# Optimization experiments

Measured on AMD Instinct MI355X. Metric: run time of the kernel, lower is better.

## Reference

```python
import jax, jax.numpy as jnp
import numpy as np

FACTOR = 5.0
SCALE = 1.0 / np.sqrt(FACTOR)  # module uses scale or 1/sqrt(factor), NOT 1/sqrt(E)


def setup_inputs() -> dict:
    key = jax.random.key(0)
    k1, k2, k3, k4 = jax.random.split(key, 4)
    B, H, L, S, E = 8, 8, 1024, 1024, 64
    queries = jax.random.normal(k1, (B, H, L, E), dtype=jnp.float32)
    keys = jax.random.normal(k2, (B, H, S, E), dtype=jnp.float32)
    values = jax.random.normal(k3, (B, H, S, E), dtype=jnp.float32)
    time_diffs = jax.random.uniform(k4, (B, L), dtype=jnp.float32)  # non-negative time gaps
    return {"queries": queries, "keys": keys, "values": values, "time_diffs": time_diffs}


def reference(queries, keys, values, time_diffs):
    # decay: [B, 1, L, 1] multiplicative bias on raw scores (pre-scale, pre-softmax)
    decay = jnp.exp(-time_diffs / FACTOR)[:, None, :, None]
    scores = jnp.einsum('bhle,bhse->bhls', queries, keys) * decay  # [B,H,L,S]
    A = jax.nn.softmax(SCALE * scores, axis=-1)
    V = jnp.einsum('bhls,bhse->bhle', A, values)
    return V
```

## Files before the change

kernel.cpp:

```cpp
#include <hip/hip_runtime.h>
#include <hip/hip_bf16.h>


#define Lq   1024
#define Sk   1024
#define Ed   64
#define QBLK 128
#define KVBLK 64
#define NT   (Sk / KVBLK)
#define NBH  64

typedef __attribute__((ext_vector_type(8)))  short          short8;
typedef __attribute__((ext_vector_type(8)))  unsigned short ushort8;
typedef __attribute__((ext_vector_type(4)))  float          f32x4;
typedef __attribute__((ext_vector_type(16))) float          f32x16;
typedef __attribute__((ext_vector_type(4)))  unsigned int   uint4v;

__device__ __forceinline__ unsigned short f2bf(float x) {
    unsigned int u = __float_as_uint(x);
    u += 0x7FFFu + ((u >> 16) & 1u);
    return (unsigned short)(u >> 16);
}

__device__ __forceinline__ unsigned cvt_pk_bf16(float lo, float hi) {
    unsigned r;
    asm("v_cvt_pk_bf16_f32 %0, %1, %2" : "=v"(r) : "v"(lo), "v"(hi));
    return r;
}

__device__ __forceinline__ void gl_lds16(const void* g, void* lds) {
    __builtin_amdgcn_global_load_lds(
        (const __attribute__((address_space(1))) void*)g,
        (__attribute__((address_space(3))) void*)lds, 16, 0, 0);
}

__global__ __launch_bounds__(256) void prep_kv(const float* __restrict__ K,
                                               const float* __restrict__ V,
                                               unsigned short* __restrict__ Kb,
                                               unsigned short* __restrict__ Vt) {
    int bid = blockIdx.x;
    if (bid < 2048) {
        int gid = bid * 256 + threadIdx.x;
        int row = gid >> 3;
        int jb  = gid & 7;
        const float* src = K + (size_t)row * Ed + jb * 8;
        float4 a = *(const float4*)src;
        float4 c = *(const float4*)(src + 4);
        ushort8 w;
        w[0]=f2bf(a.x); w[1]=f2bf(a.y); w[2]=f2bf(a.z); w[3]=f2bf(a.w);
        w[4]=f2bf(c.x); w[5]=f2bf(c.y); w[6]=f2bf(c.z); w[7]=f2bf(c.w);
        *(ushort8*)(Kb + (size_t)row * Ed + ((jb ^ (row & 7)) << 3)) = w;
    } else {
        int vb  = bid - 2048;
        int bh  = vb >> 4;
        int kv0 = (vb & 15) * KVBLK;
        int e   = threadIdx.x & 63;
        int jh  = threadIdx.x >> 6;
        const float* Vg = V + (size_t)bh * Sk * Ed;
        unsigned short* Vo = Vt + (size_t)bh * Ed * Sk;
        #pragma unroll
        for (int half = 0; half < 2; ++half) {
            int jb = jh + half * 4;
            ushort8 w;
            #pragma unroll
            for (int i = 0; i < 8; ++i)
                w[i] = f2bf(Vg[(size_t)(kv0 + jb * 8 + i) * Ed + e]);
            *(ushort8*)(Vo + (size_t)e * Sk + kv0 + ((jb ^ (e & 7)) << 3)) = w;
        }
    }
}

__global__ __launch_bounds__(256, 2) void ta_attn7(
    const float* __restrict__ Q, const float* __restrict__ TD,
    const unsigned short* __restrict__ Kb, const unsigned short* __restrict__ Vt,
    float* __restrict__ O)
{
    __shared__ __align__(16) unsigned short Kl[2][KVBLK][Ed];
    __shared__ __align__(16) unsigned short Vl[2][Ed][KVBLK];

    const int d    = blockIdx.x;
    const int wg   = (d & 7) * 64 + (d >> 3);
    const int bh   = wg >> 3;
    const int qb   = wg & 7;
    const int b    = bh >> 3;
    const int tid  = threadIdx.x;
    const int wave = tid >> 6, lane = tid & 63;
    const int ln31 = lane & 31;
    const int hi   = lane >> 5;
    const int l7   = ln31 & 7;

    const char* KbBH = (const char*)(Kb + (size_t)bh * Sk * Ed);
    const char* VtBH = (const char*)(Vt + (size_t)bh * Ed * Sk);
    const int q0w = qb * QBLK + wave * 32;

    {
        char* kd = (char*)&Kl[0][0][0];
        char* vd = (char*)&Vl[0][0][0];
        #pragma unroll
        for (int p = 0; p < 2; ++p) {
            unsigned o_ = tid * 16 + p * 4096;
            gl_lds16(KbBH + o_, kd + o_);
            unsigned e = o_ >> 7, c = o_ & 127;
            gl_lds16(VtBH + (size_t)e * 2048 + c, vd + o_);
        }
    }

    const float SCALE = 0.44721359549995793f;
    const float LOG2E = 1.4426950408889634f;
    const float rscale = SCALE * LOG2E * __expf(-TD[b * Lq + q0w + ln31] * 0.2f);
    short8 qa[4];
    {
        const float* qp = Q + ((size_t)bh * Lq + q0w + ln31) * Ed + hi * 8;
        #pragma unroll
        for (int kc = 0; kc < 4; ++kc) {
            float4 a = *(const float4*)(qp + kc * 16);
            float4 c = *(const float4*)(qp + kc * 16 + 4);
            ushort8 t;
            t[0]=f2bf(a.x*rscale); t[1]=f2bf(a.y*rscale);
            t[2]=f2bf(a.z*rscale); t[3]=f2bf(a.w*rscale);
            t[4]=f2bf(c.x*rscale); t[5]=f2bf(c.y*rscale);
            t[6]=f2bf(c.z*rscale); t[7]=f2bf(c.w*rscale);
            qa[kc] = __builtin_bit_cast(short8, t);
        }
    }

    float sum = 0.f;
    f32x16 o[2];
    #pragma unroll
    for (int eb = 0; eb < 2; ++eb)
        #pragma unroll
        for (int i = 0; i < 16; ++i) o[eb][i] = 0.f;

    int cur = 0;
    for (int t = 0; t < NT; ++t) {
        __syncthreads();
        if (t + 1 < NT) {
            char* kd = (char*)&Kl[cur ^ 1][0][0];
            char* vd = (char*)&Vl[cur ^ 1][0][0];
            #pragma unroll
            for (int p = 0; p < 2; ++p) {
                unsigned o_ = tid * 16 + p * 4096;
                gl_lds16(KbBH + (size_t)(t + 1) * 8192 + o_, kd + o_);
                unsigned e = o_ >> 7, c = o_ & 127;
                gl_lds16(VtBH + (size_t)e * 2048 + (size_t)(t + 1) * 128 + c, vd + o_);
            }
        }

        f32x16 s[2];
        __builtin_amdgcn_s_setprio(1);
        #pragma unroll
        for (int kvb = 0; kvb < 2; ++kvb) {
            #pragma unroll
            for (int i = 0; i < 16; ++i) s[kvb][i] = 0.f;
            #pragma unroll
            for (int kc = 0; kc < 4; ++kc) {
                ushort8 kr = *(const ushort8*)((const char*)&Kl[cur][0][0]
                    + (kvb * 32 + ln31) * 128 + (((2 * kc + hi) ^ l7) << 4));
                s[kvb] = __builtin_amdgcn_mfma_f32_32x32x16_bf16(
                    __builtin_bit_cast(short8, kr), qa[kc], s[kvb], 0, 0, 0);
            }
        }
        __builtin_amdgcn_s_setprio(0);

        unsigned w[2][4][2];
        #pragma unroll
        for (int kvb = 0; kvb < 2; ++kvb)
            #pragma unroll
            for (int mp = 0; mp < 4; ++mp) {
                float p0 = exp2f(s[kvb][4 * mp + 0]);
                float p1 = exp2f(s[kvb][4 * mp + 1]);
                float p2 = exp2f(s[kvb][4 * mp + 2]);
                float p3 = exp2f(s[kvb][4 * mp + 3]);
                sum += (p0 + p1) + (p2 + p3);
                w[kvb][mp][0] = cvt_pk_bf16(p0, p1);
                w[kvb][mp][1] = cvt_pk_bf16(p2, p3);
            }

        short8 pa[4];
        #pragma unroll
        for (int ks = 0; ks < 4; ++ks) {
            const int kvb = ks >> 1, mm = ks & 1;
            unsigned a0 = w[kvb][2 * mm][0], b0 = w[kvb][2 * mm + 1][0];
            unsigned a1 = w[kvb][2 * mm][1], b1 = w[kvb][2 * mm + 1][1];
            asm volatile("v_permlane32_swap_b32 %0, %1" : "+v"(a0), "+v"(b0));
            asm volatile("v_permlane32_swap_b32 %0, %1" : "+v"(a1), "+v"(b1));
            uint4v u; u[0] = a0; u[1] = a1; u[2] = b0; u[3] = b1;
            pa[ks] = __builtin_bit_cast(short8, u);
        }

        __builtin_amdgcn_s_setprio(1);
        #pragma unroll
        for (int eb = 0; eb < 2; ++eb)
            #pragma unroll
            for (int ks = 0; ks < 4; ++ks) {
                ushort8 vr = *(const ushort8*)((const char*)&Vl[cur][0][0]
                    + (eb * 32 + ln31) * 128 + (((2 * ks + hi) ^ l7) << 4));
                o[eb] = __builtin_amdgcn_mfma_f32_32x32x16_bf16(
                    pa[ks], __builtin_bit_cast(short8, vr), o[eb], 0, 0, 0);
            }
        __builtin_amdgcn_s_setprio(0);
        cur ^= 1;
    }

    float stot = sum + __shfl_xor(sum, 32);
    float* Og = O + (size_t)bh * Lq * Ed;
    #pragma unroll
    for (int r = 0; r < 16; ++r) {
        const int qrow = (r & 3) + 8 * (r >> 2) + 4 * hi;
        float inv = 1.0f / __shfl(stot, qrow);
        float* op = Og + (size_t)(q0w + qrow) * Ed + ln31;
        op[0]  = o[0][r] * inv;
        op[32] = o[1][r] * inv;
    }
}

__global__ __launch_bounds__(256, 2) void ta_attn_fb(
    const float* __restrict__ Q, const float* __restrict__ K,
    const float* __restrict__ V, const float* __restrict__ TD,
    float* __restrict__ O)
{
    __shared__ __align__(16) unsigned short Kl[32][72];
    __shared__ __align__(16) unsigned short Vt[Ed][40];
    __shared__ __align__(16) unsigned short Pl[4][16][40];

    const int bid  = blockIdx.x;
    const int bh   = bid >> 4;
    const int qb   = bid & 15;
    const int b    = bh >> 3;
    const int tid  = threadIdx.x;
    const int wave = tid >> 6, lane = tid & 63;
    const int lg   = lane >> 4;
    const int ln   = lane & 15;

    const float* Qg = Q + (size_t)bh * Lq * Ed;
    const float* Kg = K + (size_t)bh * Sk * Ed;
    const float* Vg = V + (size_t)bh * Sk * Ed;
    const int q0 = qb * 64 + wave * 16;

    short8 qa[2];
    {
        const float* qp = Qg + (size_t)(q0 + ln) * Ed + lg * 8;
        for (int ks = 0; ks < 2; ++ks) {
            float4 a = *(const float4*)(qp + ks * 32);
            float4 c = *(const float4*)(qp + ks * 32 + 4);
            ushort8 t2;
            t2[0]=f2bf(a.x); t2[1]=f2bf(a.y); t2[2]=f2bf(a.z); t2[3]=f2bf(a.w);
            t2[4]=f2bf(c.x); t2[5]=f2bf(c.y); t2[6]=f2bf(c.z); t2[7]=f2bf(c.w);
            qa[ks] = __builtin_bit_cast(short8, t2);
        }
    }

    const float SCALE = 0.44721359549995793f;
    float rs[4], m[4], sum[4];
    for (int r = 0; r < 4; ++r) {
        int row = q0 + lg * 4 + r;
        rs[r]  = SCALE * __expf(-TD[b * Lq + row] * 0.2f);
        m[r]   = -1e30f;
        sum[r] = 0.f;
    }
    f32x4 o[4];
    for (int eb = 0; eb < 4; ++eb) o[eb] = (f32x4){0.f, 0.f, 0.f, 0.f};

    const int srow = tid >> 3;
    const int scol = (tid & 7) * 8;

    for (int t = 0; t < 32; ++t) {
        const int kv0 = t * 32;
        __syncthreads();
        {
            const float* kp = Kg + (size_t)(kv0 + srow) * Ed + scol;
            float4 a = *(const float4*)kp;
            float4 c = *(const float4*)(kp + 4);
            ushort8 tk;
            tk[0]=f2bf(a.x); tk[1]=f2bf(a.y); tk[2]=f2bf(a.z); tk[3]=f2bf(a.w);
            tk[4]=f2bf(c.x); tk[5]=f2bf(c.y); tk[6]=f2bf(c.z); tk[7]=f2bf(c.w);
            *(ushort8*)&Kl[srow][scol] = tk;
            const float* vp = Vg + (size_t)(kv0 + srow) * Ed + scol;
            float4 va = *(const float4*)vp;
            float4 vc = *(const float4*)(vp + 4);
            float vv[8] = {va.x,va.y,va.z,va.w,vc.x,vc.y,vc.z,vc.w};
            #pragma unroll
            for (int i = 0; i < 8; ++i) Vt[scol + i][srow] = f2bf(vv[i]);
        }
        __syncthreads();

        f32x4 s[2];
        #pragma unroll
        for (int cb = 0; cb < 2; ++cb) {
            s[cb] = (f32x4){0.f, 0.f, 0.f, 0.f};
            #pragma unroll
            for (int ks = 0; ks < 2; ++ks) {
                ushort8 kraw = *(const ushort8*)&Kl[cb*16 + ln][lg*8 + ks*32];
                s[cb] = __builtin_amdgcn_mfma_f32_16x16x32_bf16(
                    qa[ks], __builtin_bit_cast(short8, kraw), s[cb], 0, 0, 0);
            }
        }
        #pragma unroll
        for (int r = 0; r < 4; ++r) {
            float s0 = s[0][r] * rs[r];
            float s1 = s[1][r] * rs[r];
            float tm = fmaxf(s0, s1);
            tm = fmaxf(tm, __shfl_xor(tm, 1));
            tm = fmaxf(tm, __shfl_xor(tm, 2));
            tm = fmaxf(tm, __shfl_xor(tm, 4));
            tm = fmaxf(tm, __shfl_xor(tm, 8));
            float mn   = fmaxf(m[r], tm);
            float corr = __expf(m[r] - mn);
            m[r] = mn;
            float p0 = __expf(s0 - mn);
            float p1 = __expf(s1 - mn);
            float ts = p0 + p1;
            ts += __shfl_xor(ts, 1);
            ts += __shfl_xor(ts, 2);
            ts += __shfl_xor(ts, 4);
            ts += __shfl_xor(ts, 8);
            sum[r] = sum[r] * corr + ts;
            #pragma unroll
            for (int eb = 0; eb < 4; ++eb) o[eb][r] *= corr;
            Pl[wave][lg*4 + r][ln]      = f2bf(p0);
            Pl[wave][lg*4 + r][16 + ln] = f2bf(p1);
        }
        ushort8 praw = *(const ushort8*)&Pl[wave][ln][lg*8];
        short8  pa   = __builtin_bit_cast(short8, praw);
        #pragma unroll
        for (int eb = 0; eb < 4; ++eb) {
            ushort8 vraw = *(const ushort8*)&Vt[eb*16 + ln][lg*8];
            o[eb] = __builtin_amdgcn_mfma_f32_16x16x32_bf16(
                pa, __builtin_bit_cast(short8, vraw), o[eb], 0, 0, 0);
        }
    }

    float* Og = O + (size_t)bh * Lq * Ed;
    #pragma unroll
    for (int r = 0; r < 4; ++r) {
        float inv = 1.0f / sum[r];
        int row = q0 + lg * 4 + r;
        #pragma unroll
        for (int eb = 0; eb < 4; ++eb)
            Og[(size_t)row * Ed + eb*16 + ln] = o[eb][r] * inv;
    }
}

extern "C" void kernel_launch(void* const* d_in, const int* in_sizes, int n_in,
                              void* d_out, int out_size, void* d_ws, size_t ws_size,
                              hipStream_t stream) {
    const float* Q  = (const float*)d_in[0];
    const float* K  = (const float*)d_in[1];
    const float* V  = (const float*)d_in[2];
    const float* TD = (const float*)d_in[3];
    float* O = (float*)d_out;

    const size_t elems = (size_t)NBH * Sk * Ed;
    const size_t need  = 2 * elems * sizeof(unsigned short);

    if (ws_size >= need) {
        unsigned short* Kb = (unsigned short*)d_ws;
        unsigned short* Vt = Kb + elems;
        prep_kv<<<dim3(3072), dim3(256), 0, stream>>>(K, V, Kb, Vt);
        ta_attn7<<<dim3(NBH * (Lq / QBLK)), dim3(256), 0, stream>>>(Q, TD, Kb, Vt, O);
    } else {
        ta_attn_fb<<<dim3(NBH * 16), dim3(256), 0, stream>>>(Q, K, V, TD, O);
    }
}
```

Baseline: 52.37 us.

## Split KV loop across two wave groups per block with LDS reduction

Doubles the block to 512 threads, with each group of four waves processing half of the key/value tiles into its own double-buffered LDS region. Partial output accumulators and row sums from the second half are written to shared memory and added by the first half before normalization and store. This aims to raise wave-level parallelism and shorten the serial KV loop per wave, at the cost of more LDS per block, an extra cross-wave reduction and additional barriers.

```diff
diff --git a/kernel.cpp b/kernel.cpp
--- a/kernel.cpp
+++ b/kernel.cpp
@@ -7,7 +7,7 @@
 #define Ed   64
 #define QBLK 128
 #define KVBLK 64
-#define NT   (Sk / KVBLK)
+#define NTH  8
 #define NBH  64
 
 typedef __attribute__((ext_vector_type(8)))  short          short8;
@@ -70,13 +70,12 @@
     }
 }
 
-__global__ __launch_bounds__(256, 2) void ta_attn7(
+__global__ __launch_bounds__(512, 4) void ta_attn8(
     const float* __restrict__ Q, const float* __restrict__ TD,
     const unsigned short* __restrict__ Kb, const unsigned short* __restrict__ Vt,
     float* __restrict__ O)
 {
-    __shared__ __align__(16) unsigned short Kl[2][KVBLK][Ed];
-    __shared__ __align__(16) unsigned short Vl[2][Ed][KVBLK];
+    __shared__ __align__(16) char smem[65536];
 
     const int d    = blockIdx.x;
     const int wg   = (d & 7) * 64 + (d >> 3);
@@ -85,23 +84,27 @@
     const int b    = bh >> 3;
     const int tid  = threadIdx.x;
     const int wave = tid >> 6, lane = tid & 63;
+    const int half = wave >> 2, qw = wave & 3;
     const int ln31 = lane & 31;
     const int hi   = lane >> 5;
     const int l7   = ln31 & 7;
+    const int st   = tid & 255;
 
     const char* KbBH = (const char*)(Kb + (size_t)bh * Sk * Ed);
     const char* VtBH = (const char*)(Vt + (size_t)bh * Ed * Sk);
-    const int q0w = qb * QBLK + wave * 32;
+    const int q0w = qb * QBLK + qw * 32;
+
+    char* baseK = smem + half * 32768;
+    char* baseV = baseK + 16384;
 
     {
-        char* kd = (char*)&Kl[0][0][0];
-        char* vd = (char*)&Vl[0][0][0];
+        const size_t tg = (size_t)(half * NTH);
         #pragma unroll
         for (int p = 0; p < 2; ++p) {
-            unsigned o_ = tid * 16 + p * 4096;
-            gl_lds16(KbBH + o_, kd + o_);
+            unsigned o_ = st * 16 + p * 4096;
+            gl_lds16(KbBH + tg * 8192 + o_, baseK + o_);
             unsigned e = o_ >> 7, c = o_ & 127;
-            gl_lds16(VtBH + (size_t)e * 2048 + c, vd + o_);
+            gl_lds16(VtBH + (size_t)e * 2048 + tg * 128 + c, baseV + o_);
         }
     }
 
@@ -132,19 +135,22 @@
         for (int i = 0; i < 16; ++i) o[eb][i] = 0.f;
 
     int cur = 0;
-    for (int t = 0; t < NT; ++t) {
+    for (int tt = 0; tt < NTH; ++tt) {
         __syncthreads();
-        if (t + 1 < NT) {
-            char* kd = (char*)&Kl[cur ^ 1][0][0];
-            char* vd = (char*)&Vl[cur ^ 1][0][0];
+        if (tt + 1 < NTH) {
+            const size_t tg = (size_t)(half * NTH + tt + 1);
+            char* kd = baseK + (cur ^ 1) * 8192;
+            char* vd = baseV + (cur ^ 1) * 8192;
             #pragma unroll
             for (int p = 0; p < 2; ++p) {
-                unsigned o_ = tid * 16 + p * 4096;
-                gl_lds16(KbBH + (size_t)(t + 1) * 8192 + o_, kd + o_);
+                unsigned o_ = st * 16 + p * 4096;
+                gl_lds16(KbBH + tg * 8192 + o_, kd + o_);
                 unsigned e = o_ >> 7, c = o_ & 127;
-                gl_lds16(VtBH + (size_t)e * 2048 + (size_t)(t + 1) * 128 + c, vd + o_);
-            }
-        }
+                gl_lds16(VtBH + (size_t)e * 2048 + tg * 128 + c, vd + o_);
+            }
+        }
+        const char* kb = baseK + cur * 8192;
+        const char* vb = baseV + cur * 8192;
 
         f32x16 s[2];
         __builtin_amdgcn_s_setprio(1);
@@ -154,7 +160,7 @@
             for (int i = 0; i < 16; ++i) s[kvb][i] = 0.f;
             #pragma unroll
             for (int kc = 0; kc < 4; ++kc) {
-                ushort8 kr = *(const ushort8*)((const char*)&Kl[cur][0][0]
+                ushort8 kr = *(const ushort8*)(kb
                     + (kvb * 32 + ln31) * 128 + (((2 * kc + hi) ^ l7) << 4));
                 s[kvb] = __builtin_amdgcn_mfma_f32_32x32x16_bf16(
                     __builtin_bit_cast(short8, kr), qa[kc], s[kvb], 0, 0, 0);
@@ -193,7 +199,7 @@
         for (int eb = 0; eb < 2; ++eb)
             #pragma unroll
             for (int ks = 0; ks < 4; ++ks) {
-                ushort8 vr = *(const ushort8*)((const char*)&Vl[cur][0][0]
+                ushort8 vr = *(const ushort8*)(vb
                     + (eb * 32 + ln31) * 128 + (((2 * ks + hi) ^ l7) << 4));
                 o[eb] = __builtin_amdgcn_mfma_f32_32x32x16_bf16(
                     pa[ks], __builtin_bit_cast(short8, vr), o[eb], 0, 0, 0);
@@ -202,15 +208,40 @@
         cur ^= 1;
     }
 
-    float stot = sum + __shfl_xor(sum, 32);
-    float* Og = O + (size_t)bh * Lq * Ed;
-    #pragma unroll
-    for (int r = 0; r < 16; ++r) {
-        const int qrow = (r & 3) + 8 * (r >> 2) + 4 * hi;
-        float inv = 1.0f / __shfl(stot, qrow);
-        float* op = Og + (size_t)(q0w + qrow) * Ed + ln31;
-        op[0]  = o[0][r] * inv;
-        op[32] = o[1][r] * inv;
+    __syncthreads();
+    float* Lo = (float*)smem;
+    float* Ls = (float*)(smem + 32768);
+    if (half == 1) {
+        Ls[qw * 64 + lane] = sum + __shfl_xor(sum, 32);
+        #pragma unroll
+        for (int eb = 0; eb < 2; ++eb)
+            #pragma unroll
+            for (int c4 = 0; c4 < 4; ++c4) {
+                f32x4 v = { o[eb][c4*4+0], o[eb][c4*4+1],
+                            o[eb][c4*4+2], o[eb][c4*4+3] };
+                *(f32x4*)(Lo + qw * 2048 + (eb * 4 + c4) * 256 + lane * 4) = v;
+            }
+    }
+    __syncthreads();
+    if (half == 0) {
+        float stot = sum + __shfl_xor(sum, 32) + Ls[qw * 64 + lane];
+        #pragma unroll
+        for (int eb = 0; eb < 2; ++eb)
+            #pragma unroll
+            for (int c4 = 0; c4 < 4; ++c4) {
+                f32x4 v = *(const f32x4*)(Lo + qw * 2048 + (eb * 4 + c4) * 256 + lane * 4);
+                o[eb][c4*4+0] += v[0]; o[eb][c4*4+1] += v[1];
+                o[eb][c4*4+2] += v[2]; o[eb][c4*4+3] += v[3];
+            }
+        float* Og = O + (size_t)bh * Lq * Ed;
+        #pragma unroll
+        for (int r = 0; r < 16; ++r) {
+            const int qrow = (r & 3) + 8 * (r >> 2) + 4 * hi;
+            float inv = 1.0f / __shfl(stot, qrow);
+            float* op = Og + (size_t)(q0w + qrow) * Ed + ln31;
+            op[0]  = o[0][r] * inv;
+            op[32] = o[1][r] * inv;
+        }
     }
 }
 
@@ -357,7 +388,7 @@
         unsigned short* Kb = (unsigned short*)d_ws;
         unsigned short* Vt = Kb + elems;
         prep_kv<<<dim3(3072), dim3(256), 0, stream>>>(K, V, Kb, Vt);
-        ta_attn7<<<dim3(NBH * (Lq / QBLK)), dim3(256), 0, stream>>>(Q, TD, Kb, Vt, O);
+        ta_attn8<<<dim3(NBH * (Lq / QBLK)), dim3(512), 0, stream>>>(Q, TD, Kb, Vt, O);
     } else {
         ta_attn_fb<<<dim3(NBH * 16), dim3(256), 0, stream>>>(Q, K, V, TD, O);
     }
```

After: 49.48 us. 1.06x faster.
